# Performance work log

Measured on AMD Instinct MI355X. Metric: run time of the kernel, lower is better.

The kernel has to match this reference:

```python
import jax, jax.numpy as jnp
import numpy as np

C, H_IMG = 1, 1024
N_PATCH = 64
L = 12          # blocks
NH = 12         # heads
D = 768         # hidden_d
DH = D // NH    # head dim
MLP = 4 * D
OUT_D = 1000
BATCH = 256
PATCH = H_IMG // N_PATCH
IN_D = C * PATCH
SEQ = N_PATCH + 1


def _pos_emb(pos, dim):
    # faithful to original: exponent uses i directly (2*i/dim), sin for even i, cos for odd i
    p = np.arange(pos, dtype=np.float64)[:, None]
    i = np.arange(dim, dtype=np.float64)[None, :]
    ang = p / np.power(10000.0, 2.0 * i / dim)
    pe = np.where((np.arange(dim)[None, :] % 2) == 0, np.sin(ang), np.cos(ang))
    return jnp.asarray(pe, dtype=jnp.float32)


def setup_inputs() -> dict:
    key = jax.random.key(0)
    ks = jax.random.split(key, 24)
    s = lambda fan: 1.0 / np.sqrt(fan)
    inp = {
        "images": jax.random.normal(ks[0], (BATCH, C, H_IMG), jnp.float32),
        "linear_w": jax.random.uniform(ks[1], (D, IN_D), jnp.float32, -s(IN_D), s(IN_D)),
        "linear_b": jax.random.uniform(ks[2], (D,), jnp.float32, -s(IN_D), s(IN_D)),
        "class_token": jax.random.uniform(ks[3], (1, D), jnp.float32),
        "pos_emb": _pos_emb(SEQ, D),
        "ln1_g": jnp.ones((L, D), jnp.float32),
        "ln1_b": jnp.zeros((L, D), jnp.float32),
        "wq": jax.random.uniform(ks[4], (L, NH, DH, DH), jnp.float32, -s(DH), s(DH)),
        "bq": jax.random.uniform(ks[5], (L, NH, DH), jnp.float32, -s(DH), s(DH)),
        "wk": jax.random.uniform(ks[6], (L, NH, DH, DH), jnp.float32, -s(DH), s(DH)),
        "bk": jax.random.uniform(ks[7], (L, NH, DH), jnp.float32, -s(DH), s(DH)),
        "wv": jax.random.uniform(ks[8], (L, NH, DH, DH), jnp.float32, -s(DH), s(DH)),
        "bv": jax.random.uniform(ks[9], (L, NH, DH), jnp.float32, -s(DH), s(DH)),
        "ln2_g": jnp.ones((L, D), jnp.float32),
        "ln2_b": jnp.zeros((L, D), jnp.float32),
        "w1": jax.random.uniform(ks[10], (L, MLP, D), jnp.float32, -s(D), s(D)),
        "b1": jax.random.uniform(ks[11], (L, MLP), jnp.float32, -s(D), s(D)),
        "w2": jax.random.uniform(ks[12], (L, D, MLP), jnp.float32, -s(MLP), s(MLP)),
        "b2": jax.random.uniform(ks[13], (L, D), jnp.float32, -s(MLP), s(MLP)),
        "head_w": jax.random.uniform(ks[14], (OUT_D, D), jnp.float32, -s(D), s(D)),
        "head_b": jax.random.uniform(ks[15], (OUT_D,), jnp.float32, -s(D), s(D)),
    }
    return inp


def _ln(x, g, b):
    m = jnp.mean(x, axis=-1, keepdims=True)
    v = jnp.var(x, axis=-1, keepdims=True)
    return (x - m) / jnp.sqrt(v + 1e-5) * g + b


def _block(x, g1, be1, wq, bq, wk, bk, wv, bv, g2, be2, w1, bb1, w2, bb2):
    B, S, _ = x.shape
    h = _ln(x, g1, be1).reshape(B, S, NH, DH)  # split heads along feature dim
    q = jnp.einsum('bshd,hed->bshe', h, wq) + bq
    k = jnp.einsum('bshd,hed->bshe', h, wk) + bk
    v = jnp.einsum('bshd,hed->bshe', h, wv) + bv
    scores = jnp.einsum('bshe,bthe->bhst', q, k) / np.sqrt(DH).astype(np.float32)
    attn = jax.nn.softmax(scores, axis=-1)
    o = jnp.einsum('bhst,bthe->bshe', attn, v).reshape(B, S, D)
    x = x + o
    h2 = _ln(x, g2, be2)
    m = jax.nn.gelu(jnp.einsum('bsd,fd->bsf', h2, w1) + bb1, approximate=False)
    m = jnp.einsum('bsf,df->bsd', m, w2) + bb2
    return x + m


def reference(images, linear_w, linear_b, class_token, pos_emb,
              ln1_g, ln1_b, wq, bq, wk, bk, wv, bv, ln2_g, ln2_b,
              w1, b1, w2, b2, head_w, head_b):
    n = images.shape[0]
    # patchify: [n, c, h] -> [n, n_patch, c*patch_size] (flatten is (c, patch) row-major)
    patches = images.reshape(n, C, N_PATCH, PATCH).transpose(0, 2, 1, 3).reshape(n, N_PATCH, IN_D)
    tokens = jnp.einsum('npi,di->npd', patches, linear_w) + linear_b
    cls = jnp.broadcast_to(class_token[None], (n, 1, D))
    x = jnp.concatenate([cls, tokens], axis=1) + pos_emb[None]
    for l in range(L):
        x = _block(x, ln1_g[l], ln1_b[l], wq[l], bq[l], wk[l], bk[l], wv[l], bv[l],
                   ln2_g[l], ln2_b[l], w1[l], b1[l], w2[l], b2[l])
    cls_out = x[:, 0]
    logits = cls_out @ head_w.T + head_b
    return jax.nn.softmax(logits, axis=-1)
```

## Files before the change

kernel.cpp:

```cpp
#include <hip/hip_runtime.h>

#define NLAYER 12
#define NHEAD  12
#define DHEAD  64
#define DMODEL 768
#define SEQL   65
#define NBATCH 256
#define MTOK   (NBATCH*SEQL)
#define MLPD   3072

typedef _Float16 f16;
typedef f16  f16x8 __attribute__((ext_vector_type(8)));
typedef f16  f16x4 __attribute__((ext_vector_type(4)));
typedef float f32x4 __attribute__((ext_vector_type(4)));

#define MFMA(a,b,c) __builtin_amdgcn_mfma_f32_16x16x32_f16(a,b,c,0,0,0)

__device__ __forceinline__ void gload16(const void* g, void* l) {
  __builtin_amdgcn_global_load_lds((const __attribute__((address_space(1))) void*)g,
                                   (__attribute__((address_space(3))) void*)l, 16, 0, 0);
}

__global__ __launch_bounds__(256) void cvt_f16k(const float* __restrict__ in,
                                                f16* __restrict__ out, int n) {
  long i = ((long)blockIdx.x*256 + threadIdx.x)*4;
  if (i >= n) return;
  const float4 v = *(const float4*)(in + i);
  f16x4 o = { (f16)v.x, (f16)v.y, (f16)v.z, (f16)v.w };
  *(f16x4*)(out + i) = o;
}

__global__ __launch_bounds__(256) void patch_embed(
    const float* __restrict__ images, const float* __restrict__ lw,
    const float* __restrict__ lb, const float* __restrict__ cls,
    const float* __restrict__ pe, float* __restrict__ x) {
  const int s = blockIdx.x, n = blockIdx.y, tid = threadIdx.x;
  __shared__ float p[16];
  if (s > 0 && tid < 16) p[tid] = images[(long)n*1024 + (s-1)*16 + tid];
  __syncthreads();
  float* xr = x + ((long)n*SEQL + s)*DMODEL;
  #pragma unroll
  for (int j = 0; j < 3; ++j) {
    int d = tid + j*256;
    float v;
    if (s == 0) {
      v = cls[d] + pe[d];
    } else {
      float acc = lb[d];
      #pragma unroll
      for (int i = 0; i < 16; ++i) acc += p[i]*lw[d*16+i];
      v = acc + pe[s*DMODEL + d];
    }
    xr[d] = v;
  }
}

__global__ __launch_bounds__(256) void ln_kernel(
    const float* __restrict__ x, const float* __restrict__ g,
    const float* __restrict__ b, f16* __restrict__ out) {
  const int row = blockIdx.x, tid = threadIdx.x;
  const float* xr = x + (long)row*DMODEL;
  float v0 = xr[tid], v1 = xr[tid+256], v2 = xr[tid+512];
  float s = v0+v1+v2;
  float s2 = v0*v0 + v1*v1 + v2*v2;
  #pragma unroll
  for (int o = 32; o >= 1; o >>= 1) { s += __shfl_xor(s, o); s2 += __shfl_xor(s2, o); }
  __shared__ float red[8];
  const int wave = tid>>6, lane = tid&63;
  if (lane == 0) { red[wave] = s; red[4+wave] = s2; }
  __syncthreads();
  s  = red[0]+red[1]+red[2]+red[3];
  s2 = red[4]+red[5]+red[6]+red[7];
  float mean = s * (1.f/768.f);
  float var  = s2 * (1.f/768.f) - mean*mean;
  float rstd = rsqrtf(var + 1e-5f);
  f16* orow = out + (long)row*DMODEL;
  orow[tid]     = (f16)((v0-mean)*rstd*g[tid]     + b[tid]);
  orow[tid+256] = (f16)((v1-mean)*rstd*g[tid+256] + b[tid+256]);
  orow[tid+512] = (f16)((v2-mean)*rstd*g[tid+512] + b[tid+512]);
}

__global__ __launch_bounds__(256) void attn_kernel(
    const f16* __restrict__ h, const f16* __restrict__ wq, const f16* __restrict__ wk,
    const f16* __restrict__ wv, const float* __restrict__ bq, const float* __restrict__ bk,
    const float* __restrict__ bv, float* __restrict__ x) {
  __shared__ __align__(16) f16 HsPs[80*104];
  __shared__ __align__(16) f16 Qs[80*72];
  __shared__ __align__(16) f16 Ks[80*72];
  __shared__ __align__(16) f16 Vt[64*104];
  const int hd = blockIdx.x, b = blockIdx.y;
  const int tid = threadIdx.x, wave = tid>>6, lane = tid&63;
  const int lc = lane & 15, lg = lane >> 4;
  const f16* hbase = h + ((long)b*SEQL)*DMODEL + hd*DHEAD;

  for (int c = tid; c < 80*8; c += 256) {
    int s = c >> 3, ec = (c & 7)*8;
    uint4 val = {0u,0u,0u,0u};
    if (s < SEQL) val = *(const uint4*)(hbase + (long)s*DMODEL + ec);
    *(uint4*)&HsPs[s*104 + ec] = val;
  }
  for (int c = tid; c < 64*104/8; c += 256) {
    uint4 z = {0u,0u,0u,0u};
    *(uint4*)&Vt[c*8] = z;
  }
  __syncthreads();

  for (int task = wave; task < 15; task += 4) {
    int mat = task / 5, mt = task % 5;
    const f16* W = (mat == 0 ? wq : mat == 1 ? wk : wv) + hd*DHEAD*DHEAD;
    const float* bias = (mat == 0 ? bq : mat == 1 ? bk : bv) + hd*DHEAD;
    #pragma unroll
    for (int nt = 0; nt < 4; ++nt) {
      f32x4 a = {0.f,0.f,0.f,0.f};
      #pragma unroll
      for (int kt = 0; kt < 2; ++kt) {
        f16x8 af = *(const f16x8*)&HsPs[(mt*16 + lc)*104 + kt*32 + lg*8];
        f16x8 bf = *(const f16x8*)&W[(nt*16 + lc)*DHEAD + kt*32 + lg*8];
        a = MFMA(af, bf, a);
      }
      float bb = bias[nt*16 + lc];
      #pragma unroll
      for (int r = 0; r < 4; ++r) {
        int s = mt*16 + lg*4 + r;
        int e = nt*16 + lc;
        float v = a[r] + bb;
        if (mat == 0)      Qs[s*72 + e] = (f16)v;
        else if (mat == 1) Ks[s*72 + e] = (f16)v;
        else               Vt[e*104 + s] = (f16)v;
      }
    }
  }
  __syncthreads();

  for (int mt = wave; mt < 5; mt += 4) {
    {
      uint2 z = {0u,0u};
      *(uint2*)&HsPs[(mt*16 + (lane>>2))*104 + 80 + (lane&3)*4] = z;
    }
    f32x4 sc[5];
    #pragma unroll
    for (int nt = 0; nt < 5; ++nt) {
      f32x4 a = {0.f,0.f,0.f,0.f};
      #pragma unroll
      for (int kt = 0; kt < 2; ++kt) {
        f16x8 af = *(const f16x8*)&Qs[(mt*16 + lc)*72 + kt*32 + lg*8];
        f16x8 bf = *(const f16x8*)&Ks[(nt*16 + lc)*72 + kt*32 + lg*8];
        a = MFMA(af, bf, a);
      }
      sc[nt] = a;
    }
    #pragma unroll
    for (int r = 0; r < 4; ++r) {
      float vals[5];
      #pragma unroll
      for (int nt = 0; nt < 5; ++nt) {
        float v = sc[nt][r]*0.125f;
        if (nt*16 + lc > 64) v = -1e30f;
        vals[nt] = v;
      }
      float mx = vals[0];
      #pragma unroll
      for (int nt = 1; nt < 5; ++nt) mx = fmaxf(mx, vals[nt]);
      #pragma unroll
      for (int o = 8; o >= 1; o >>= 1) mx = fmaxf(mx, __shfl_xor(mx, o, 16));
      float sum = 0.f, p[5];
      #pragma unroll
      for (int nt = 0; nt < 5; ++nt) { p[nt] = __expf(vals[nt]-mx); sum += p[nt]; }
      #pragma unroll
      for (int o = 8; o >= 1; o >>= 1) sum += __shfl_xor(sum, o, 16);
      float inv = 1.f/sum;
      int row = mt*16 + lg*4 + r;
      #pragma unroll
      for (int nt = 0; nt < 5; ++nt) HsPs[row*104 + nt*16 + lc] = (f16)(p[nt]*inv);
    }
    f32x4 oacc[4];
    #pragma unroll
    for (int nt = 0; nt < 4; ++nt) {
      f32x4 a = {0.f,0.f,0.f,0.f};
      #pragma unroll
      for (int kt = 0; kt < 3; ++kt) {
        f16x8 af = *(const f16x8*)&HsPs[(mt*16 + lc)*104 + kt*32 + lg*8];
        f16x8 bf = *(const f16x8*)&Vt[(nt*16 + lc)*104 + kt*32 + lg*8];
        a = MFMA(af, bf, a);
      }
      oacc[nt] = a;
    }
    float* xb = x + ((long)b*SEQL)*DMODEL + hd*DHEAD;
    #pragma unroll
    for (int nt = 0; nt < 4; ++nt) {
      #pragma unroll
      for (int r = 0; r < 4; ++r) {
        int s = mt*16 + lg*4 + r;
        if (s < SEQL) {
          int e = nt*16 + lc;
          xb[(long)s*DMODEL + e] += oacc[nt][r];
        }
      }
    }
  }
}

template<int ACT>
__global__ __launch_bounds__(256) void gemm_bt(
    const f16* __restrict__ A, const f16* __restrict__ B,
    const float* __restrict__ bias, void* __restrict__ Cout,
    int M, int N, int K) {
  __shared__ __align__(16) f16 As[128*32];
  __shared__ __align__(16) f16 Bs[128*32];
  const int tid = threadIdx.x;
  const int wave = tid >> 6, lane = tid & 63;
  const int lrow = lane & 15, lk = lane >> 4;
  const long m0 = (long)blockIdx.y * 128, n0 = (long)blockIdx.x * 128;
  const int wm = (wave >> 1) * 64, wn = (wave & 1) * 64;
  f32x4 acc[4][4];
  #pragma unroll
  for (int i = 0; i < 4; ++i)
    #pragma unroll
    for (int j = 0; j < 4; ++j) acc[i][j] = (f32x4){0.f,0.f,0.f,0.f};

  for (int k0 = 0; k0 < K; k0 += 32) {
    #pragma unroll
    for (int i = 0; i < 2; ++i) {
      int ch = (i*4 + wave)*64 + lane;
      int row = ch >> 2, kp = (ch & 3)*8;
      gload16(A + (m0 + row)*(long)K + k0 + kp, &As[ch*8]);
      gload16(B + (n0 + row)*(long)K + k0 + kp, &Bs[ch*8]);
    }
    __syncthreads();
    f16x8 af[4], bfr[4];
    #pragma unroll
    for (int i = 0; i < 4; ++i) af[i]  = *(const f16x8*)&As[(wm + i*16 + lrow)*32 + lk*8];
    #pragma unroll
    for (int j = 0; j < 4; ++j) bfr[j] = *(const f16x8*)&Bs[(wn + j*16 + lrow)*32 + lk*8];
    #pragma unroll
    for (int i = 0; i < 4; ++i)
      #pragma unroll
      for (int j = 0; j < 4; ++j)
        acc[i][j] = MFMA(af[i], bfr[j], acc[i][j]);
    __syncthreads();
  }
  #pragma unroll
  for (int j = 0; j < 4; ++j) {
    int col = (int)n0 + wn + j*16 + lrow;
    float bv = bias[col];
    #pragma unroll
    for (int i = 0; i < 4; ++i) {
      #pragma unroll
      for (int r = 0; r < 4; ++r) {
        long row = m0 + wm + i*16 + lk*4 + r;
        float v = acc[i][j][r] + bv;
        if (ACT == 0) {
          float g = 0.5f*v*(1.f + erff(v*0.70710678118654752f));
          ((f16*)Cout)[row*(long)N + col] = (f16)g;
        } else {
          ((float*)Cout)[row*(long)N + col] += v;
        }
      }
    }
  }
}

__global__ __launch_bounds__(256) void head_kernel(
    const float* __restrict__ x, const float* __restrict__ hw,
    const float* __restrict__ hb, float* __restrict__ out) {
  const int b = blockIdx.x, tid = threadIdx.x;
  __shared__ float cls[768];
  __shared__ float red[8];
  const float* xr = x + (long)b*SEQL*DMODEL;
  #pragma unroll
  for (int j = 0; j < 3; ++j) cls[tid + j*256] = xr[tid + j*256];
  __syncthreads();
  float lgv[4];
  #pragma unroll
  for (int j = 0; j < 4; ++j) {
    int c = tid + j*256;
    float acc = -1e30f;
    if (c < 1000) {
      const float* wr = hw + (long)c*768;
      float s_ = 0.f;
      for (int i = 0; i < 768; ++i) s_ += cls[i]*wr[i];
      acc = s_ + hb[c];
    }
    lgv[j] = acc;
  }
  const int wave = tid>>6, lane = tid&63;
  float mx = fmaxf(fmaxf(lgv[0],lgv[1]),fmaxf(lgv[2],lgv[3]));
  #pragma unroll
  for (int o = 32; o >= 1; o >>= 1) mx = fmaxf(mx, __shfl_xor(mx, o));
  if (lane == 0) red[wave] = mx;
  __syncthreads();
  mx = fmaxf(fmaxf(red[0],red[1]),fmaxf(red[2],red[3]));
  float e[4]; float sum = 0.f;
  #pragma unroll
  for (int j = 0; j < 4; ++j) {
    int c = tid + j*256;
    e[j] = (c < 1000) ? expf(lgv[j]-mx) : 0.f;
    sum += e[j];
  }
  #pragma unroll
  for (int o = 32; o >= 1; o >>= 1) sum += __shfl_xor(sum, o);
  if (lane == 0) red[4+wave] = sum;
  __syncthreads();
  sum = red[4]+red[5]+red[6]+red[7];
  float inv = 1.f/sum;
  #pragma unroll
  for (int j = 0; j < 4; ++j) {
    int c = tid + j*256;
    if (c < 1000) out[(long)b*1000 + c] = e[j]*inv;
  }
}

extern "C" void kernel_launch(void* const* d_in, const int* in_sizes, int n_in,
                              void* d_out, int out_size, void* d_ws, size_t ws_size,
                              hipStream_t stream) {
  const float* images     = (const float*)d_in[0];
  const float* linear_w   = (const float*)d_in[1];
  const float* linear_b   = (const float*)d_in[2];
  const float* class_tok  = (const float*)d_in[3];
  const float* pos_emb    = (const float*)d_in[4];
  const float* ln1_g      = (const float*)d_in[5];
  const float* ln1_b      = (const float*)d_in[6];
  const float* wq         = (const float*)d_in[7];
  const float* bq         = (const float*)d_in[8];
  const float* wk         = (const float*)d_in[9];
  const float* bk         = (const float*)d_in[10];
  const float* wv         = (const float*)d_in[11];
  const float* bv         = (const float*)d_in[12];
  const float* ln2_g      = (const float*)d_in[13];
  const float* ln2_b      = (const float*)d_in[14];
  const float* w1         = (const float*)d_in[15];
  const float* b1         = (const float*)d_in[16];
  const float* w2         = (const float*)d_in[17];
  const float* b2         = (const float*)d_in[18];
  const float* head_w     = (const float*)d_in[19];
  const float* head_b     = (const float*)d_in[20];

  char* ws = (char*)d_ws;
  float* xbuf = (float*)(ws + 0);
  f16*   hbuf = (f16*)(ws + 51118080);
  f16*   mbuf = (f16*)(ws + 76677120);
  f16*   w1b  = (f16*)(ws + 178913280);
  f16*   w2b  = (f16*)(ws + 183631872);
  f16*   wqb  = (f16*)(ws + 188350464);
  f16*   wkb  = (f16*)(ws + 189530112);
  f16*   wvb  = (f16*)(ws + 190709760);
  if (ws_size < 191889408ull) return;

  patch_embed<<<dim3(SEQL, NBATCH), 256, 0, stream>>>(images, linear_w, linear_b,
                                                      class_tok, pos_emb, xbuf);
  cvt_f16k<<<576, 256, 0, stream>>>(wq, wqb, 589824);
  cvt_f16k<<<576, 256, 0, stream>>>(wk, wkb, 589824);
  cvt_f16k<<<576, 256, 0, stream>>>(wv, wvb, 589824);

  for (int l = 0; l < NLAYER; ++l) {
    ln_kernel<<<MTOK, 256, 0, stream>>>(xbuf, ln1_g + l*768, ln1_b + l*768, hbuf);
    attn_kernel<<<dim3(NHEAD, NBATCH), 256, 0, stream>>>(
        hbuf, wqb + l*49152, wkb + l*49152, wvb + l*49152,
        bq + l*768, bk + l*768, bv + l*768, xbuf);
    ln_kernel<<<MTOK, 256, 0, stream>>>(xbuf, ln2_g + l*768, ln2_b + l*768, hbuf);
    cvt_f16k<<<2304, 256, 0, stream>>>(w1 + (long)l*2359296, w1b, 2359296);
    gemm_bt<0><<<dim3(MLPD/128, MTOK/128), 256, 0, stream>>>(
        hbuf, w1b, b1 + l*3072, (void*)mbuf, MTOK, MLPD, DMODEL);
    cvt_f16k<<<2304, 256, 0, stream>>>(w2 + (long)l*2359296, w2b, 2359296);
    gemm_bt<1><<<dim3(DMODEL/128, MTOK/128), 256, 0, stream>>>(
        mbuf, w2b, b2 + l*768, (void*)xbuf, MTOK, DMODEL, MLPD);
  }
  head_kernel<<<NBATCH, 256, 0, stream>>>(xbuf, head_w, head_b, (float*)d_out);
}
```

Baseline: 5.784 ms.

## Triple-buffer GEMM K loop, remap workgroups per XCD, batch weight conversion

The MLP GEMM now keeps three LDS buffers and issues global-to-LDS loads two K-steps ahead. It uses a single barrier per step, guarded by an explicit vmcnt wait, so memory latency overlaps with MFMA work. Workgroup IDs are remapped so that neighbouring tiles land on the same XCD, which should improve L2 reuse. When the workspace is large enough, all layers' W1/W2 are converted to fp16 in two big launches up front instead of two small launches per layer. The costs are triple the LDS use, which can lower occupancy, and a dependence on a larger workspace.

Result: faster. 5.434 ms (-6.0%).

```diff
diff --git a/kernel.cpp b/kernel.cpp
--- a/kernel.cpp
+++ b/kernel.cpp
@@ -205,12 +205,21 @@
     const f16* __restrict__ A, const f16* __restrict__ B,
     const float* __restrict__ bias, void* __restrict__ Cout,
     int M, int N, int K) {
-  __shared__ __align__(16) f16 As[128*32];
-  __shared__ __align__(16) f16 Bs[128*32];
+  __shared__ __align__(16) f16 As[3][128*32];
+  __shared__ __align__(16) f16 Bs[3][128*32];
   const int tid = threadIdx.x;
   const int wave = tid >> 6, lane = tid & 63;
   const int lrow = lane & 15, lk = lane >> 4;
-  const long m0 = (long)blockIdx.y * 128, n0 = (long)blockIdx.x * 128;
+
+  const int gx = gridDim.x;
+  const int nwg = gx * gridDim.y;
+  const int orig = blockIdx.y * gx + blockIdx.x;
+  const int q = nwg >> 3, r = nwg & 7;
+  const int xcd = orig & 7, lin = orig >> 3;
+  const int wgid = (xcd < r ? xcd*(q+1) : r*(q+1) + (xcd - r)*q) + lin;
+  const int bx = wgid % gx, by = wgid / gx;
+
+  const long m0 = (long)by * 128, n0 = (long)bx * 128;
   const int wm = (wave >> 1) * 64, wn = (wave & 1) * 64;
   f32x4 acc[4][4];
   #pragma unroll
@@ -218,26 +227,36 @@
     #pragma unroll
     for (int j = 0; j < 4; ++j) acc[i][j] = (f32x4){0.f,0.f,0.f,0.f};
 
-  for (int k0 = 0; k0 < K; k0 += 32) {
+  const int NT = K >> 5;
+  auto stage = [&](int slot, int t) {
+    const int k0 = t << 5;
     #pragma unroll
     for (int i = 0; i < 2; ++i) {
       int ch = (i*4 + wave)*64 + lane;
       int row = ch >> 2, kp = (ch & 3)*8;
-      gload16(A + (m0 + row)*(long)K + k0 + kp, &As[ch*8]);
-      gload16(B + (n0 + row)*(long)K + k0 + kp, &Bs[ch*8]);
-    }
-    __syncthreads();
+      gload16(A + (m0 + row)*(long)K + k0 + kp, &As[slot][ch*8]);
+      gload16(B + (n0 + row)*(long)K + k0 + kp, &Bs[slot][ch*8]);
+    }
+  };
+  stage(0, 0);
+  stage(1, 1);
+  int slot = 0;
+  for (int t = 0; t < NT; ++t) {
+    if (t < NT-1) asm volatile("s_waitcnt vmcnt(4)" ::: "memory");
+    else          asm volatile("s_waitcnt vmcnt(0)" ::: "memory");
+    asm volatile("s_barrier" ::: "memory");
+    if (t + 2 < NT) { int ns = slot + 2; if (ns >= 3) ns -= 3; stage(ns, t+2); }
     f16x8 af[4], bfr[4];
     #pragma unroll
-    for (int i = 0; i < 4; ++i) af[i]  = *(const f16x8*)&As[(wm + i*16 + lrow)*32 + lk*8];
-    #pragma unroll
-    for (int j = 0; j < 4; ++j) bfr[j] = *(const f16x8*)&Bs[(wn + j*16 + lrow)*32 + lk*8];
+    for (int i = 0; i < 4; ++i) af[i]  = *(const f16x8*)&As[slot][(wm + i*16 + lrow)*32 + lk*8];
+    #pragma unroll
+    for (int j = 0; j < 4; ++j) bfr[j] = *(const f16x8*)&Bs[slot][(wn + j*16 + lrow)*32 + lk*8];
     #pragma unroll
     for (int i = 0; i < 4; ++i)
       #pragma unroll
       for (int j = 0; j < 4; ++j)
         acc[i][j] = MFMA(af[i], bfr[j], acc[i][j]);
-    __syncthreads();
+    slot = slot + 1; if (slot >= 3) slot = 0;
   }
   #pragma unroll
   for (int j = 0; j < 4; ++j) {
@@ -246,9 +265,9 @@
     #pragma unroll
     for (int i = 0; i < 4; ++i) {
       #pragma unroll
-      for (int r = 0; r < 4; ++r) {
-        long row = m0 + wm + i*16 + lk*4 + r;
-        float v = acc[i][j][r] + bv;
+      for (int r2 = 0; r2 < 4; ++r2) {
+        long row = m0 + wm + i*16 + lk*4 + r2;
+        float v = acc[i][j][r2] + bv;
         if (ACT == 0) {
           float g = 0.5f*v*(1.f + erff(v*0.70710678118654752f));
           ((f16*)Cout)[row*(long)N + col] = (f16)g;
@@ -339,18 +358,31 @@
   float* xbuf = (float*)(ws + 0);
   f16*   hbuf = (f16*)(ws + 51118080);
   f16*   mbuf = (f16*)(ws + 76677120);
+  f16*   w1all = (f16*)(ws + 178913280);
+  f16*   w2all = (f16*)(ws + 235536384);
+  f16*   wqbB  = (f16*)(ws + 292159488);
+  f16*   wkbB  = (f16*)(ws + 293339136);
+  f16*   wvbB  = (f16*)(ws + 294518784);
   f16*   w1b  = (f16*)(ws + 178913280);
   f16*   w2b  = (f16*)(ws + 183631872);
-  f16*   wqb  = (f16*)(ws + 188350464);
-  f16*   wkb  = (f16*)(ws + 189530112);
-  f16*   wvb  = (f16*)(ws + 190709760);
+  f16*   wqbS = (f16*)(ws + 188350464);
+  f16*   wkbS = (f16*)(ws + 189530112);
+  f16*   wvbS = (f16*)(ws + 190709760);
   if (ws_size < 191889408ull) return;
+  const bool big = ws_size >= 295698432ull;
+  f16* wqb = big ? wqbB : wqbS;
+  f16* wkb = big ? wkbB : wkbS;
+  f16* wvb = big ? wvbB : wvbS;
 
   patch_embed<<<dim3(SEQL, NBATCH), 256, 0, stream>>>(images, linear_w, linear_b,
                                                       class_tok, pos_emb, xbuf);
   cvt_f16k<<<576, 256, 0, stream>>>(wq, wqb, 589824);
   cvt_f16k<<<576, 256, 0, stream>>>(wk, wkb, 589824);
   cvt_f16k<<<576, 256, 0, stream>>>(wv, wvb, 589824);
+  if (big) {
+    cvt_f16k<<<27648, 256, 0, stream>>>(w1, w1all, 28311552);
+    cvt_f16k<<<27648, 256, 0, stream>>>(w2, w2all, 28311552);
+  }
 
   for (int l = 0; l < NLAYER; ++l) {
     ln_kernel<<<MTOK, 256, 0, stream>>>(xbuf, ln1_g + l*768, ln1_b + l*768, hbuf);
@@ -358,12 +390,14 @@
         hbuf, wqb + l*49152, wkb + l*49152, wvb + l*49152,
         bq + l*768, bk + l*768, bv + l*768, xbuf);
     ln_kernel<<<MTOK, 256, 0, stream>>>(xbuf, ln2_g + l*768, ln2_b + l*768, hbuf);
-    cvt_f16k<<<2304, 256, 0, stream>>>(w1 + (long)l*2359296, w1b, 2359296);
+    f16* w1p = big ? (w1all + (long)l*2359296) : w1b;
+    f16* w2p = big ? (w2all + (long)l*2359296) : w2b;
+    if (!big) cvt_f16k<<<2304, 256, 0, stream>>>(w1 + (long)l*2359296, w1b, 2359296);
     gemm_bt<0><<<dim3(MLPD/128, MTOK/128), 256, 0, stream>>>(
-        hbuf, w1b, b1 + l*3072, (void*)mbuf, MTOK, MLPD, DMODEL);
-    cvt_f16k<<<2304, 256, 0, stream>>>(w2 + (long)l*2359296, w2b, 2359296);
+        hbuf, w1p, b1 + l*3072, (void*)mbuf, MTOK, MLPD, DMODEL);
+    if (!big) cvt_f16k<<<2304, 256, 0, stream>>>(w2 + (long)l*2359296, w2b, 2359296);
     gemm_bt<1><<<dim3(DMODEL/128, MTOK/128), 256, 0, stream>>>(
-        mbuf, w2b, b2 + l*768, (void*)xbuf, MTOK, DMODEL, MLPD);
+        mbuf, w2p, b2 + l*768, (void*)xbuf, MTOK, DMODEL, MLPD);
   }
   head_kernel<<<NBATCH, 256, 0, stream>>>(xbuf, head_w, head_b, (float*)d_out);
 }
```
